# Optimization experiments

Measured on AMD Instinct MI355X. Metric: run time of the kernel, lower is better.

## Reference

```python
import jax, jax.numpy as jnp
import numpy as np

HIDDEN_DIM = 512
SCALE = float(np.sqrt(HIDDEN_DIM))  # hidden_dim ** 0.5, matches torch


def setup_inputs() -> dict:
    key = jax.random.key(0)
    ks = jax.random.split(key, 4)
    B, S, D_IN = 8, 4096, 64
    x = jax.random.normal(ks[0], (B, S, D_IN), dtype=jnp.float32)
    # Linear weights stored as [in, out] (transposed vs torch's [out, in])
    Wq = jax.random.normal(ks[1], (D_IN, HIDDEN_DIM), dtype=jnp.float32) * (1.0 / np.sqrt(D_IN))
    Wk = jax.random.normal(ks[2], (D_IN, HIDDEN_DIM), dtype=jnp.float32) * (1.0 / np.sqrt(D_IN))
    Wv = jax.random.normal(ks[3], (D_IN, HIDDEN_DIM), dtype=jnp.float32) * (1.0 / np.sqrt(D_IN))
    bq = jnp.zeros((HIDDEN_DIM,), dtype=jnp.float32)
    bk = jnp.zeros((HIDDEN_DIM,), dtype=jnp.float32)
    bv = jnp.zeros((HIDDEN_DIM,), dtype=jnp.float32)
    return {"x": x, "Wq": Wq, "bq": bq, "Wk": Wk, "bk": bk, "Wv": Wv, "bv": bv}


def reference(x, Wq, bq, Wk, bk, Wv, bv):
    # Q/K/V projections: [B, S, H]
    Q = jnp.einsum('bsd,dh->bsh', x, Wq) + bq
    K = jnp.einsum('bsd,dh->bsh', x, Wk) + bk
    V = jnp.einsum('bsd,dh->bsh', x, Wv) + bv
    # Naive single-head attention with full [B, S, S] score matrix,
    # matching the original torch math exactly.
    scores = jnp.einsum('bqh,bkh->bqk', Q, K) / SCALE
    attn = jax.nn.softmax(scores, axis=-1)
    return jnp.einsum('bqk,bkh->bqh', attn, V)
```

## Files before the change

kernel.cpp:

```cpp
#include <hip/hip_runtime.h>
#include <hip/hip_bf16.h>
#include <math.h>


#define SS 4096
#define DD 64
#define HH 512

#define CSCALE ((float)(1.4426950408889634 * 0.04419417382415922))

typedef __bf16 bf16x8 __attribute__((ext_vector_type(8)));
typedef float  f32x4  __attribute__((ext_vector_type(4)));
typedef unsigned int u32x4 __attribute__((ext_vector_type(4)));

__device__ __forceinline__ float b2f(__hip_bfloat16 v) { return __bfloat162float(v); }

__device__ __forceinline__ f32x4 mfma16(bf16x8 a, bf16x8 b, f32x4 c) {
  return __builtin_amdgcn_mfma_f32_16x16x32_bf16(a, b, c, 0, 0, 0);
}

__device__ __forceinline__ unsigned pack2(float a, float b) {
  float2 f2; f2.x = a; f2.y = b;
  __hip_bfloat162 h2 = __float22bfloat162_rn(f2);
  unsigned u; __builtin_memcpy(&u, &h2, 4);
  return u;
}

__device__ __forceinline__ float loadf(const void* p, size_t i, int isF32) {
  return isF32 ? ((const float*)p)[i] : b2f(((const __hip_bfloat16*)p)[i]);
}
__device__ __forceinline__ void load8f(const void* p, size_t i, int isF32, float* o) {
  if (isF32) {
    const float4 a = *(const float4*)((const float*)p + i);
    const float4 b = *(const float4*)((const float*)p + i + 4);
    o[0]=a.x; o[1]=a.y; o[2]=a.z; o[3]=a.w; o[4]=b.x; o[5]=b.y; o[6]=b.z; o[7]=b.w;
  } else {
    const bf16x8 v = *(const bf16x8*)((const __hip_bfloat16*)p + i);
#pragma unroll
    for (int k = 0; k < 8; ++k) { __hip_bfloat16 h; __builtin_memcpy(&h, ((const unsigned short*)&v) + k, 2); o[k] = b2f(h); }
  }
}

__global__ void dtype_probe(const void* __restrict__ Wq, int* __restrict__ flag) {
  const unsigned short* h = (const unsigned short*)Wq;
  const int lane = threadIdx.x;
  unsigned int bits = ((unsigned int)h[lane * 2]) << 16;
  float v; __builtin_memcpy(&v, &bits, 4);
  v = fabsf(v);
  if (!isfinite(v) || v > 1e10f) v = 1e10f;
  for (int off = 1; off < 64; off <<= 1) v = fmaxf(v, __shfl_xor(v, off, 64));
  if (lane == 0) *flag = (v > 1e6f) ? 1 : 0;
}

__global__ __launch_bounds__(256) void prep_kernel(
    const void* __restrict__ Wq, const void* __restrict__ Wk,
    const void* __restrict__ Wv, const void* __restrict__ bq,
    const void* __restrict__ bk, __hip_bfloat16* __restrict__ MT,
    float* __restrict__ u, float* __restrict__ w_, float* __restrict__ c_,
    __hip_bfloat16* __restrict__ wvT, const int* __restrict__ flag) {
  const int t = threadIdx.x, blk = blockIdx.x;
  const int isF32 = *flag;
  if (blk < 64) {
    __shared__ float red[256];
    const int i = blk, j = t >> 2, part = t & 3;
    float acc = 0.f, aq[8], ak[8];
    for (int c = 0; c < 16; ++c) {
      load8f(Wq, (size_t)i * HH + part * 128 + c * 8, isF32, aq);
      load8f(Wk, (size_t)j * HH + part * 128 + c * 8, isF32, ak);
#pragma unroll
      for (int k = 0; k < 8; ++k) acc = fmaf(aq[k], ak[k], acc);
    }
    red[t] = acc;
    __syncthreads();
    if (t < 64)
      MT[t * 64 + i] = __float2bfloat16(red[t*4] + red[t*4+1] + red[t*4+2] + red[t*4+3]);
  } else if (blk == 64) {
    __shared__ float pu[256], pw[256], pc[64];
    const int i = t & 63, part = t >> 6;
    float au = 0.f, aw = 0.f, v1[8], v2[8];
    for (int c = 0; c < 16; ++c) {
      load8f(Wq, (size_t)i * HH + part * 128 + c * 8, isF32, v1);
      load8f(bk, part * 128 + c * 8, isF32, v2);
#pragma unroll
      for (int k = 0; k < 8; ++k) au = fmaf(v1[k], v2[k], au);
      load8f(Wk, (size_t)i * HH + part * 128 + c * 8, isF32, v1);
      load8f(bq, part * 128 + c * 8, isF32, v2);
#pragma unroll
      for (int k = 0; k < 8; ++k) aw = fmaf(v1[k], v2[k], aw);
    }
    pu[t] = au; pw[t] = aw;
    if (t < 64) {
      float s = 0.f;
      for (int e = 0; e < 8; ++e)
        s = fmaf(loadf(bq, t * 8 + e, isF32), loadf(bk, t * 8 + e, isF32), s);
      pc[t] = s;
    }
    __syncthreads();
    if (t < 64) {
      u[t]  = pu[t] + pu[t+64] + pu[t+128] + pu[t+192];
      w_[t] = pw[t] + pw[t+64] + pw[t+128] + pw[t+192];
    }
    if (t == 0) {
      float s = 0.f;
      for (int e = 0; e < 64; ++e) s += pc[e];
      *c_ = s;
    }
  } else {
    const int base = (blk - 65) * 2048 + t;
    for (int r = 0; r < 8; ++r) {
      const int e = base + r * 256;
      const int h = e >> 6, d = e & 63;
      wvT[e] = __float2bfloat16(loadf(Wv, (size_t)d * HH + h, isF32));
    }
  }
}

__global__ __launch_bounds__(256) void proj_kernel(
    const void* __restrict__ xraw, const __hip_bfloat16* __restrict__ MT,
    const float* __restrict__ u, const float* __restrict__ w_,
    const float* __restrict__ c_, __hip_bfloat16* __restrict__ xc,
    __hip_bfloat16* __restrict__ y, float* __restrict__ qb,
    float* __restrict__ kb, __hip_bfloat16* __restrict__ xT,
    const int* __restrict__ flag) {
  __shared__ __hip_bfloat16 xs[64 * 72];
  __shared__ __hip_bfloat16 Ms[64 * 72];
  __shared__ float us[64], wl[64];
  __shared__ float cs;

  const int t = threadIdx.x;
  const int isF32 = *flag;
  {
    const int r = t >> 2, cb = (t & 3) * 16;
    *(bf16x8*)(&Ms[r * 72 + cb])     = *(const bf16x8*)(MT + r * 64 + cb);
    *(bf16x8*)(&Ms[r * 72 + cb + 8]) = *(const bf16x8*)(MT + r * 64 + cb + 8);
  }
  if (t < 64) { us[t] = u[t]; wl[t] = w_[t]; }
  if (t == 0) cs = *c_;

  const int b = blockIdx.x & 7;
  const int sbase = (blockIdx.x >> 3) * 64;
  const int rbase = b * SS + sbase;

  for (int i = 0; i < 2; ++i) {
    const int e = i * 256 + t;
    const int row = e >> 3, col = (e & 7) * 8;
    float v[8];
    load8f(xraw, (size_t)(rbase + row) * DD + col, isF32, v);
    __hip_bfloat16* dp = xs + row * 72 + col;
#pragma unroll
    for (int k = 0; k < 8; ++k) dp[k] = __float2bfloat16(v[k]);
  }
  __syncthreads();

  const int wv = t >> 6, lane = t & 63;
  const int l16 = lane & 15, quad = lane >> 4;
  const bf16x8 A0 = *(const bf16x8*)(&xs[(wv * 16 + l16) * 72 + quad * 8]);
  const bf16x8 A1 = *(const bf16x8*)(&xs[(wv * 16 + l16) * 72 + 32 + quad * 8]);
#pragma unroll
  for (int nt = 0; nt < 4; ++nt) {
    const bf16x8 B0 = *(const bf16x8*)(&Ms[(nt * 16 + l16) * 72 + quad * 8]);
    const bf16x8 B1 = *(const bf16x8*)(&Ms[(nt * 16 + l16) * 72 + 32 + quad * 8]);
    f32x4 C = (f32x4){0.f, 0.f, 0.f, 0.f};
    C = mfma16(A0, B0, C);
    C = mfma16(A1, B1, C);
#pragma unroll
    for (int r = 0; r < 4; ++r)
      y[(size_t)(rbase + wv * 16 + quad * 4 + r) * DD + nt * 16 + l16] =
          __float2bfloat16(C[r]);
  }
  if (t < 64) {
    float qa = 0.f, ka = 0.f;
    for (int d = 0; d < 64; ++d) {
      const float xv = b2f(xs[t * 72 + d]);
      qa = fmaf(xv, us[d], qa);
      ka = fmaf(xv, wl[d], ka);
    }
    qb[rbase + t] = (qa + cs) * CSCALE;
    kb[rbase + t] = ka * CSCALE;
  }
  for (int i = 0; i < 2; ++i) {
    const int e = i * 256 + t;
    const int row = e >> 3, col = (e & 7) * 8;
    *(bf16x8*)(xc + (size_t)(rbase + row) * DD + col) = *(const bf16x8*)(xs + row * 72 + col);
  }
  for (int i = 0; i < 16; ++i) {
    const int d = i * 4 + (t >> 6);
    const int sl = t & 63;
    xT[((size_t)b * DD + d) * SS + sbase + sl] = xs[sl * 72 + d];
  }
}

__global__ __launch_bounds__(256) void attn_kernel(
    const __hip_bfloat16* __restrict__ x,
    const __hip_bfloat16* __restrict__ y,
    const float* __restrict__ qb, const float* __restrict__ kb,
    const __hip_bfloat16* __restrict__ xT,
    const __hip_bfloat16* __restrict__ wvT,
    const void* __restrict__ bv_raw,
    void* __restrict__ out_raw, const int* __restrict__ flag) {
  __shared__ __hip_bfloat16 xs[2][32 * 72];
  __shared__ __hip_bfloat16 vsm[2][64 * 40];
  __shared__ float kbl[SS];
  const int tid = threadIdx.x;
  const int wv = tid >> 6, lane = tid & 63;
  const int l16 = lane & 15, quad = lane >> 4;
  const int b = blockIdx.x & 7;
  const int qt = (blockIdx.x >> 3) * 4 + wv;
  const size_t rowq = ((size_t)b << 12) + ((size_t)qt << 4);
  const int isF32 = *flag;

  const __hip_bfloat16* xb  = x  + ((size_t)b * SS) * DD;
  const __hip_bfloat16* xTb = xT + ((size_t)b * DD) * SS;
  const float* kbb = kb + ((size_t)b * SS);

  const __hip_bfloat16* yp = y + (rowq + l16) * DD + quad * 8;
  const bf16x8 Ylo = *(const bf16x8*)yp;
  const bf16x8 Yhi = *(const bf16x8*)(yp + 32);
  const float qbl = qb[rowq + l16];

  const int sxr = tid >> 3, sxc = (tid & 7) * 8;
  const int svd = tid >> 2, svc = (tid & 3) * 8;
  const __hip_bfloat16* gx = xb + (size_t)sxr * DD + sxc;
  const __hip_bfloat16* gv = xTb + (size_t)svd * SS + svc;

#pragma unroll
  for (int j = 0; j < 4; ++j) {
    const int c = j * 256 + tid;
    *(f32x4*)(&kbl[c * 4]) = *(const f32x4*)(kbb + c * 4);
  }

  bf16x8 nx = *(const bf16x8*)gx;
  bf16x8 nv = *(const bf16x8*)gv;
  *(bf16x8*)(&xs[0][sxr * 72 + sxc]) = nx;
  *(bf16x8*)(&vsm[0][svd * 40 + svc]) = nv;
  nx = *(const bf16x8*)(gx + 32 * DD);
  nv = *(const bf16x8*)(gv + 32);
  __syncthreads();

  bf16x8 onesb;
#pragma unroll
  for (int j = 0; j < 8; ++j) onesb[j] = (__bf16)1.0f;

  f32x4 O[4];
#pragma unroll
  for (int n = 0; n < 4; ++n) O[n] = (f32x4){0.f, 0.f, 0.f, 0.f};
  f32x4 Ol = (f32x4){0.f, 0.f, 0.f, 0.f};

  const int rA = 8 * (l16 >> 2) + (l16 & 3);

  for (int kt = 0; kt < SS; kt += 32) {
    const int p = (kt >> 5) & 1, np = p ^ 1;
    if (kt + 32 < SS) {
      *(bf16x8*)(&xs[np][sxr * 72 + sxc]) = nx;
      *(bf16x8*)(&vsm[np][svd * 40 + svc]) = nv;
      if (kt + 64 < SS) {
        nx = *(const bf16x8*)(gx + (size_t)(kt + 64) * DD);
        nv = *(const bf16x8*)(gv + (kt + 64));
      }
    }

    const bf16x8 B00 = *(const bf16x8*)(&xs[p][rA * 72 + quad * 8]);
    const bf16x8 B01 = *(const bf16x8*)(&xs[p][rA * 72 + 32 + quad * 8]);
    const bf16x8 B10 = *(const bf16x8*)(&xs[p][(rA + 4) * 72 + quad * 8]);
    const bf16x8 B11 = *(const bf16x8*)(&xs[p][(rA + 4) * 72 + 32 + quad * 8]);
    const bf16x8 V0 = *(const bf16x8*)(&vsm[p][l16 * 40 + quad * 8]);
    const bf16x8 V1 = *(const bf16x8*)(&vsm[p][(16 + l16) * 40 + quad * 8]);
    const bf16x8 V2 = *(const bf16x8*)(&vsm[p][(32 + l16) * 40 + quad * 8]);
    const bf16x8 V3 = *(const bf16x8*)(&vsm[p][(48 + l16) * 40 + quad * 8]);

    f32x4 S0 = (f32x4){0.f, 0.f, 0.f, 0.f};
    f32x4 S1 = (f32x4){0.f, 0.f, 0.f, 0.f};
    S0 = mfma16(B00, Ylo, S0);
    S0 = mfma16(B01, Yhi, S0);
    S1 = mfma16(B10, Ylo, S1);
    S1 = mfma16(B11, Yhi, S1);

    const f32x4 kb0 = *(const f32x4*)(&kbl[kt + quad * 8]);
    const f32x4 kb1 = *(const f32x4*)(&kbl[kt + quad * 8 + 4]);

    float p0[4], p1[4];
#pragma unroll
    for (int r = 0; r < 4; ++r) {
      p0[r] = __builtin_amdgcn_exp2f(fmaf(S0[r], CSCALE, qbl + kb0[r]));
      p1[r] = __builtin_amdgcn_exp2f(fmaf(S1[r], CSCALE, qbl + kb1[r]));
    }
    u32x4 R;
    R[0] = pack2(p0[0], p0[1]);
    R[1] = pack2(p0[2], p0[3]);
    R[2] = pack2(p1[0], p1[1]);
    R[3] = pack2(p1[2], p1[3]);
    bf16x8 Pf;
    __builtin_memcpy(&Pf, &R, 16);

    O[0] = mfma16(Pf, V0, O[0]);
    O[1] = mfma16(Pf, V1, O[1]);
    O[2] = mfma16(Pf, V2, O[2]);
    O[3] = mfma16(Pf, V3, O[3]);
    Ol = mfma16(Pf, onesb, Ol);

    __syncthreads();
  }

  float inv_l[4];
#pragma unroll
  for (int r = 0; r < 4; ++r)
    inv_l[r] = (Ol[r] > 0.f) ? 1.0f / Ol[r] : 0.f;
  __hip_bfloat16* pl = &xs[0][0] + wv * 1152;
#pragma unroll
  for (int n = 0; n < 4; ++n)
#pragma unroll
    for (int r = 0; r < 4; ++r) {
      const int row = quad * 4 + r;
      pl[row * 72 + n * 16 + l16] = __float2bfloat16(O[n][r] * inv_l[r]);
    }
  __syncthreads();
  const bf16x8 Alo = *(const bf16x8*)(pl + l16 * 72 + quad * 8);
  const bf16x8 Ahi = *(const bf16x8*)(pl + l16 * 72 + 32 + quad * 8);

  float* outf = (float*)out_raw;
  __hip_bfloat16* outb = (__hip_bfloat16*)out_raw;
#pragma unroll 4
  for (int ht = 0; ht < 32; ++ht) {
    const __hip_bfloat16* wp = wvT + (size_t)(ht * 16 + l16) * DD + quad * 8;
    const bf16x8 Wlo = *(const bf16x8*)wp;
    const bf16x8 Whi = *(const bf16x8*)(wp + 32);
    f32x4 C = (f32x4){0.f, 0.f, 0.f, 0.f};
    C = mfma16(Alo, Wlo, C);
    C = mfma16(Ahi, Whi, C);
    const float bvv = loadf(bv_raw, ht * 16 + l16, isF32);
#pragma unroll
    for (int r = 0; r < 4; ++r) {
      const size_t oidx = (rowq + quad * 4 + r) * HH + ht * 16 + l16;
      const float val = C[r] + bvv;
      if (isF32) outf[oidx] = val;
      else       outb[oidx] = __float2bfloat16(val);
    }
  }
}

extern "C" void kernel_launch(void* const* d_in, const int* in_sizes, int n_in,
                              void* d_out, int out_size, void* d_ws,
                              size_t ws_size, hipStream_t stream) {
  char* ws = (char*)d_ws;
  int*   flag = (int*)(ws + 0);
  __hip_bfloat16* MT = (__hip_bfloat16*)(ws + 1024);
  float* u    = (float*)(ws + 9216);
  float* w_   = (float*)(ws + 9728);
  float* c_   = (float*)(ws + 10240);
  __hip_bfloat16* wvT = (__hip_bfloat16*)(ws + 32768);
  __hip_bfloat16* xc  = (__hip_bfloat16*)(ws + 131072);
  __hip_bfloat16* y   = (__hip_bfloat16*)(ws + 4325376);
  float* qb = (float*)(ws + 8519680);
  float* kb = (float*)(ws + 8650752);
  __hip_bfloat16* xT = (__hip_bfloat16*)(ws + 8781824);

  dtype_probe<<<1, 64, 0, stream>>>(d_in[1], flag);
  prep_kernel<<<81, 256, 0, stream>>>(d_in[1], d_in[3], d_in[5], d_in[2],
                                      d_in[4], MT, u, w_, c_, wvT, flag);
  proj_kernel<<<512, 256, 0, stream>>>(d_in[0], MT, u, w_, c_, xc, y, qb, kb,
                                       xT, flag);
  attn_kernel<<<512, 256, 0, stream>>>(xc, y, qb, kb, xT, wvT, d_in[6], d_out,
                                       flag);
}
```

Baseline: 191.0 us.

## Load V fragments directly from global into registers and pre-permute x rows in LDS

Drops the LDS staging buffer for the transposed x (V operand). Each wave now loads its MFMA V fragments straight from global memory into registers, prefetching one tile ahead. The x tile is written to LDS with a permuted row index at store time, so the read side uses simple contiguous row addressing. This cuts LDS traffic and footprint and removes index math from the inner loop. In exchange, every wave redundantly reads the same V data from global or L2 instead of sharing it through LDS, and register pressure rises.

```diff
diff --git a/kernel.cpp b/kernel.cpp
--- a/kernel.cpp
+++ b/kernel.cpp
@@ -199,7 +199,6 @@
     const void* __restrict__ bv_raw,
     void* __restrict__ out_raw, const int* __restrict__ flag) {
   __shared__ __hip_bfloat16 xs[2][32 * 72];
-  __shared__ __hip_bfloat16 vsm[2][64 * 40];
   __shared__ float kbl[SS];
   const int tid = threadIdx.x;
   const int wv = tid >> 6, lane = tid & 63;
@@ -219,9 +218,12 @@
   const float qbl = qb[rowq + l16];
 
   const int sxr = tid >> 3, sxc = (tid & 7) * 8;
-  const int svd = tid >> 2, svc = (tid & 3) * 8;
+  const int taur = (sxr & 3) + ((sxr >> 3) << 2) + (((sxr >> 2) & 1) << 4);
   const __hip_bfloat16* gx = xb + (size_t)sxr * DD + sxc;
-  const __hip_bfloat16* gv = xTb + (size_t)svd * SS + svc;
+  __hip_bfloat16* const stp = &xs[0][0] + taur * 72 + sxc;
+  const int bufel = 32 * 72;
+
+  const __hip_bfloat16* gv = xTb + (size_t)l16 * SS + quad * 8;
 
 #pragma unroll
   for (int j = 0; j < 4; ++j) {
@@ -230,11 +232,12 @@
   }
 
   bf16x8 nx = *(const bf16x8*)gx;
-  bf16x8 nv = *(const bf16x8*)gv;
-  *(bf16x8*)(&xs[0][sxr * 72 + sxc]) = nx;
-  *(bf16x8*)(&vsm[0][svd * 40 + svc]) = nv;
+  *(bf16x8*)stp = nx;
   nx = *(const bf16x8*)(gx + 32 * DD);
-  nv = *(const bf16x8*)(gv + 32);
+  bf16x8 V0n = *(const bf16x8*)(gv);
+  bf16x8 V1n = *(const bf16x8*)(gv + 16 * SS);
+  bf16x8 V2n = *(const bf16x8*)(gv + 32 * SS);
+  bf16x8 V3n = *(const bf16x8*)(gv + 48 * SS);
   __syncthreads();
 
   bf16x8 onesb;
@@ -245,28 +248,24 @@
 #pragma unroll
   for (int n = 0; n < 4; ++n) O[n] = (f32x4){0.f, 0.f, 0.f, 0.f};
   f32x4 Ol = (f32x4){0.f, 0.f, 0.f, 0.f};
-
-  const int rA = 8 * (l16 >> 2) + (l16 & 3);
 
   for (int kt = 0; kt < SS; kt += 32) {
     const int p = (kt >> 5) & 1, np = p ^ 1;
     if (kt + 32 < SS) {
-      *(bf16x8*)(&xs[np][sxr * 72 + sxc]) = nx;
-      *(bf16x8*)(&vsm[np][svd * 40 + svc]) = nv;
-      if (kt + 64 < SS) {
-        nx = *(const bf16x8*)(gx + (size_t)(kt + 64) * DD);
-        nv = *(const bf16x8*)(gv + (kt + 64));
-      }
-    }
-
-    const bf16x8 B00 = *(const bf16x8*)(&xs[p][rA * 72 + quad * 8]);
-    const bf16x8 B01 = *(const bf16x8*)(&xs[p][rA * 72 + 32 + quad * 8]);
-    const bf16x8 B10 = *(const bf16x8*)(&xs[p][(rA + 4) * 72 + quad * 8]);
-    const bf16x8 B11 = *(const bf16x8*)(&xs[p][(rA + 4) * 72 + 32 + quad * 8]);
-    const bf16x8 V0 = *(const bf16x8*)(&vsm[p][l16 * 40 + quad * 8]);
-    const bf16x8 V1 = *(const bf16x8*)(&vsm[p][(16 + l16) * 40 + quad * 8]);
-    const bf16x8 V2 = *(const bf16x8*)(&vsm[p][(32 + l16) * 40 + quad * 8]);
-    const bf16x8 V3 = *(const bf16x8*)(&vsm[p][(48 + l16) * 40 + quad * 8]);
+      *(bf16x8*)(stp + np * bufel) = nx;
+      if (kt + 64 < SS) nx = *(const bf16x8*)(gx + (size_t)(kt + 64) * DD);
+    }
+    const bf16x8 V0 = V0n, V1 = V1n, V2 = V2n, V3 = V3n;
+    const int ktn = (kt + 32 < SS) ? (kt + 32) : 0;
+    V0n = *(const bf16x8*)(gv + ktn);
+    V1n = *(const bf16x8*)(gv + 16 * SS + ktn);
+    V2n = *(const bf16x8*)(gv + 32 * SS + ktn);
+    V3n = *(const bf16x8*)(gv + 48 * SS + ktn);
+
+    const bf16x8 B00 = *(const bf16x8*)(&xs[p][l16 * 72 + quad * 8]);
+    const bf16x8 B01 = *(const bf16x8*)(&xs[p][l16 * 72 + 32 + quad * 8]);
+    const bf16x8 B10 = *(const bf16x8*)(&xs[p][(16 + l16) * 72 + quad * 8]);
+    const bf16x8 B11 = *(const bf16x8*)(&xs[p][(16 + l16) * 72 + 32 + quad * 8]);
 
     f32x4 S0 = (f32x4){0.f, 0.f, 0.f, 0.f};
     f32x4 S1 = (f32x4){0.f, 0.f, 0.f, 0.f};
```

Result: slower. 248.6 us (+30.2%).
